# Kernel optimization log

Measured on AMD Instinct MI355X. Metric: run time of the kernel, lower is better.

The kernel has to match this reference:

```python
import jax, jax.numpy as jnp
import numpy as np

S = 4096            # num tokens (single causal sequence)
HID = 1024          # hidden_size
NH = 16             # num query heads
NKV = 4             # num kv heads
HD = 64             # head_dim
THETA = 10000.0
Q_SIZE = NH * HD
KV_SIZE = NKV * HD


def setup_inputs() -> dict:
    key = jax.random.key(0)
    k1, k2, k3 = jax.random.split(key, 3)
    return {
        "positions": jnp.arange(S, dtype=jnp.int32),
        "hidden_states": jax.random.normal(k1, (S, 2 * HID), dtype=jnp.float32),
        "w_qkv": jax.random.normal(k2, (Q_SIZE + 2 * KV_SIZE, 2 * HID), dtype=jnp.float32) * 0.02,
        "w_o": jax.random.normal(k3, (HID, Q_SIZE), dtype=jnp.float32) * 0.02,
    }


def _rope(x, positions):
    # x: [S, H, HD]; neox-style rotate-half RoPE
    half = HD // 2
    inv_freq = 1.0 / (THETA ** (jnp.arange(0, half, dtype=jnp.float32) / half))
    freqs = positions.astype(jnp.float32)[:, None] * inv_freq  # [S, half]
    cos = jnp.cos(freqs)[:, None, :]  # [S, 1, half]
    sin = jnp.sin(freqs)[:, None, :]
    x1, x2 = x[..., :half], x[..., half:]
    return jnp.concatenate([x1 * cos - x2 * sin, x2 * cos + x1 * sin], axis=-1)


def reference(positions, hidden_states, w_qkv, w_o):
    qkv = hidden_states @ w_qkv.T  # [S, Q_SIZE + 2*KV_SIZE]
    q = qkv[:, :Q_SIZE].reshape(S, NH, HD)
    k = qkv[:, Q_SIZE:Q_SIZE + KV_SIZE].reshape(S, NKV, HD)
    v = qkv[:, Q_SIZE + KV_SIZE:].reshape(S, NKV, HD)
    q = _rope(q, positions)
    k = _rope(k, positions)
    # GQA: group query heads over kv heads
    g = NH // NKV
    qg = q.reshape(S, NKV, g, HD)
    scale = HD ** -0.5
    scores = jnp.einsum("qhgd,thd->hgqt", qg, k) * scale  # [NKV, g, S, S]
    causal = positions[:, None] >= positions[None, :]      # [S, S]
    scores = jnp.where(causal[None, None], scores, jnp.finfo(scores.dtype).min)
    probs = jax.nn.softmax(scores, axis=-1)
    o = jnp.einsum("hgqt,thd->qhgd", probs, v).reshape(S, Q_SIZE)
    return o @ w_o.T  # [S, HID]
```

## Files before the change

### kernel.cpp

```cpp
#include <hip/hip_runtime.h>
#include <math.h>

#define S_LEN   4096
#define NHEADS  16
#define NKVH    4
#define HDIM    64
#define QKV_N   1536
#define HID2    2048
#define OUT_N   1024

typedef __attribute__((ext_vector_type(8))) __bf16 bf16x8;
typedef __attribute__((ext_vector_type(4))) __bf16 bf16x4;
typedef __attribute__((ext_vector_type(4))) float  f32x4;
typedef __attribute__((ext_vector_type(16))) float f32x16;
typedef __attribute__((ext_vector_type(4))) unsigned int u32x4;

#define GL_LDS16(gaddr, laddr)                                                  \
  __builtin_amdgcn_global_load_lds(                                             \
      (const __attribute__((address_space(1))) unsigned int*)(gaddr),           \
      (__attribute__((address_space(3))) unsigned int*)(laddr), 16, 0, 0)

__device__ __forceinline__ unsigned cvt_pk_bf16(float lo, float hi) {
  unsigned r;
  asm("v_cvt_pk_bf16_f32 %0, %1, %2" : "=v"(r) : "v"(lo), "v"(hi));
  return r;
}

#define CVT_BLOCKS 6144
__global__ __launch_bounds__(256) void cvt_all(const float* __restrict__ hid,
                                               const float* __restrict__ wq,
                                               const float* __restrict__ wo,
                                               const int* __restrict__ positions,
                                               __bf16* __restrict__ hid_bf,
                                               __bf16* __restrict__ wq_bf,
                                               __bf16* __restrict__ wo_bf,
                                               float* __restrict__ ct,
                                               float* __restrict__ st) {
  if (blockIdx.x < CVT_BLOCKS) {
    const int n1 = S_LEN * HID2;
    const int n2 = QKV_N * HID2;
    int i = (blockIdx.x * blockDim.x + threadIdx.x) * 8;
    const float* src; __bf16* dst; int off;
    if (i < n1)           { src = hid; dst = hid_bf; off = i; }
    else if (i < n1 + n2) { src = wq;  dst = wq_bf;  off = i - n1; }
    else                  { src = wo;  dst = wo_bf;  off = i - n1 - n2; }
    float4 a = *(const float4*)(src + off);
    float4 b = *(const float4*)(src + off + 4);
    bf16x8 o = {(__bf16)a.x,(__bf16)a.y,(__bf16)a.z,(__bf16)a.w,
                (__bf16)b.x,(__bf16)b.y,(__bf16)b.z,(__bf16)b.w};
    *(bf16x8*)(dst + off) = o;
  } else {
    int i = (blockIdx.x - CVT_BLOCKS) * blockDim.x + threadIdx.x;
    int s = i >> 5, d = i & 31;
    double inv = pow(10000.0, -(double)d / 32.0);
    double fr = (double)positions[s] * inv;
    ct[i] = (float)cos(fr);
    st[i] = (float)sin(fr);
  }
}

template<int BM, bool C_BF16>
__global__ __launch_bounds__(256) void gemm_m97(const __bf16* __restrict__ A,
                                                const __bf16* __restrict__ B,
                                                void* __restrict__ Cp,
                                                int M, int N, int K) {
  constexpr int TM = BM / 32;
  __shared__ __align__(16) __bf16 As[BM * 32];
  __shared__ __align__(16) __bf16 Bs[128 * 32];
  const int tid  = threadIdx.x;
  const int bm   = blockIdx.x, bn = blockIdx.y;
  const int wave = tid >> 6, lane = tid & 63;
  const int quad = lane >> 4, col = lane & 15;
  const int wm = (wave >> 1) * (BM / 2), wn = (wave & 1) * 64;

  const int lrow = lane >> 2, lcol = (lane & 3) * 8;
  const __bf16* Ag = A + (size_t)(bm * BM + wave * (BM / 4) + lrow) * K + lcol;
  const __bf16* Bg = B + (size_t)(bn * 128 + wave * 32 + lrow) * K + lcol;
  __bf16* AsW = As + wave * (BM / 4) * 32;
  __bf16* BsW = Bs + wave * 32 * 32;

  f32x4 acc[TM][4];
#pragma unroll
  for (int i = 0; i < TM; ++i)
#pragma unroll
    for (int j = 0; j < 4; ++j) acc[i][j] = (f32x4){0.f, 0.f, 0.f, 0.f};

  for (int kk = 0; kk < K; kk += 32) {
    __syncthreads();
#pragma unroll
    for (int u = 0; u < BM / 64; ++u)
      GL_LDS16(Ag + kk + (size_t)(u * 16) * K, AsW + u * 16 * 32);
    GL_LDS16(Bg + kk,                  BsW);
    GL_LDS16(Bg + kk + (size_t)16 * K, BsW + 16 * 32);
    __syncthreads();

    bf16x8 a[TM], b[4];
#pragma unroll
    for (int tm = 0; tm < TM; ++tm)
      a[tm] = *(const bf16x8*)&As[(wm + tm * 16 + col) * 32 + quad * 8];
#pragma unroll
    for (int tn = 0; tn < 4; ++tn)
      b[tn] = *(const bf16x8*)&Bs[(wn + tn * 16 + col) * 32 + quad * 8];
#pragma unroll
    for (int tm = 0; tm < TM; ++tm)
#pragma unroll
      for (int tn = 0; tn < 4; ++tn)
        acc[tm][tn] = __builtin_amdgcn_mfma_f32_16x16x32_bf16(a[tm], b[tn], acc[tm][tn], 0, 0, 0);
  }

#pragma unroll
  for (int tm = 0; tm < TM; ++tm)
#pragma unroll
    for (int tn = 0; tn < 4; ++tn) {
      int row = bm * BM + wm + tm * 16 + quad * 4;
      int cg  = bn * 128 + wn + tn * 16 + col;
#pragma unroll
      for (int r = 0; r < 4; ++r) {
        if constexpr (C_BF16)
          ((__bf16*)Cp)[(size_t)(row + r) * N + cg] = (__bf16)acc[tm][tn][r];
        else
          ((float*)Cp)[(size_t)(row + r) * N + cg] = acc[tm][tn][r];
      }
    }
}

#define RC_BLOCKS 320
__global__ __launch_bounds__(256) void rope_cast_vt(const __bf16* __restrict__ qkv,
                                                    const float* __restrict__ ct,
                                                    const float* __restrict__ st,
                                                    __bf16* __restrict__ qb,
                                                    __bf16* __restrict__ kb,
                                                    __bf16* __restrict__ vT) {
  if (blockIdx.x < RC_BLOCKS) {
    int g = blockIdx.x * 256 + threadIdx.x;
    int head = g % 20, s = g / 20;
    bool isq = head < NHEADS;
    const __bf16* src = qkv + (size_t)s * QKV_N +
                        (isq ? head * 64 : 1024 + (head - 16) * 64);
    bf16x8 x[8];
#pragma unroll
    for (int u = 0; u < 8; ++u) x[u] = *(const bf16x8*)(src + u * 8);
    float cc[32], ss[32];
#pragma unroll
    for (int u = 0; u < 8; ++u) {
      float4 c4 = *(const float4*)(ct + s * 32 + u * 4);
      float4 s4 = *(const float4*)(st + s * 32 + u * 4);
      cc[4*u] = c4.x; cc[4*u+1] = c4.y; cc[4*u+2] = c4.z; cc[4*u+3] = c4.w;
      ss[4*u] = s4.x; ss[4*u+1] = s4.y; ss[4*u+2] = s4.z; ss[4*u+3] = s4.w;
    }
    const float scl = isq ? 0.18033688011112042f : 1.0f;
    bf16x8 o[8];
#pragma unroll
    for (int d = 0; d < 32; ++d) {
      float x1 = (float)x[d >> 3][d & 7];
      float x2 = (float)x[4 + (d >> 3)][d & 7];
      o[d >> 3][d & 7]       = (__bf16)((x1 * cc[d] - x2 * ss[d]) * scl);
      o[4 + (d >> 3)][d & 7] = (__bf16)((x2 * cc[d] + x1 * ss[d]) * scl);
    }
    __bf16* dst = isq ? (qb + (size_t)s * 1024 + head * 64)
                      : (kb + (size_t)s * 256 + (head - 16) * 64);
#pragma unroll
    for (int u = 0; u < 8; ++u) *(bf16x8*)(dst + u * 8) = o[u];
  } else {
    __shared__ __align__(16) __bf16 Ts[64][72];
    const int idx = blockIdx.x - RC_BLOCKS;
    const int sb = idx & 63, kvh = idx >> 6, t = threadIdx.x;
    const int r = t >> 2, c16 = (t & 3) * 16;
    const __bf16* src = qkv + (size_t)(sb * 64 + r) * QKV_N + 1280 + kvh * 64 + c16;
    bf16x8 v0 = *(const bf16x8*)src;
    bf16x8 v1 = *(const bf16x8*)(src + 8);
#pragma unroll
    for (int u = 0; u < 8; ++u) {
      Ts[c16 + u][r]     = v0[u];
      Ts[c16 + 8 + u][r] = v1[u];
    }
    __syncthreads();
    __bf16* dst = vT + ((size_t)kvh * 64 + r) * S_LEN + sb * 64 + c16;
    *(bf16x8*)dst       = *(const bf16x8*)&Ts[r][c16];
    *(bf16x8*)(dst + 8) = *(const bf16x8*)&Ts[r][c16 + 8];
  }
}

__global__ __launch_bounds__(256, 4) void attn_split(const __bf16* __restrict__ qg,
                                                     const __bf16* __restrict__ kg,
                                                     const __bf16* __restrict__ vg,
                                                     __bf16* __restrict__ op0,
                                                     __bf16* __restrict__ op1,
                                                     __bf16* __restrict__ op2,
                                                     __bf16* __restrict__ op3,
                                                     float* __restrict__ lp) {
  __shared__ __align__(16) __bf16 lds[18432];
  __bf16* Ks = lds;
  __bf16* Vs = lds + 9216;

  const int tid = threadIdx.x;
  const int h = blockIdx.x;
  const int y = 79 - (int)blockIdx.y;
  int qb, c;
  if (y < 8)       { qb = y;                 c = 0; }
  else if (y < 24) { qb = 8  + ((y - 8) >> 1);  c = (y - 8) & 1; }
  else if (y < 48) { qb = 16 + (y - 24) / 3;    c = (y - 24) % 3; }
  else             { qb = 24 + ((y - 48) >> 2); c = (y - 48) & 3; }
  const int n   = 2 * (qb + 1);
  const int nch = (qb >> 3) + 1;
  const int bsz = n / nch, rm = n - bsz * nch;
  const int kt0 = c * bsz + (c < rm ? c : rm);
  const int ktEnd = kt0 + bsz + (c < rm ? 1 : 0);

  const int kvh = h >> 2;
  const int wave = tid >> 6, lane = tid & 63;
  const int r31 = lane & 31, hi = lane >> 5;
  const int hi4 = hi * 4, hi8 = hi * 8;
  const int qbase = qb * 128 + wave * 32;

  {
    const int r = tid >> 1, cc = (tid & 1) * 32;
    const __bf16* src = qg + (size_t)(qb * 128 + r) * 1024 + h * 64 + cc;
    __bf16* dq = lds + r * 72 + cc;
    *(bf16x8*)(dq)      = *(const bf16x8*)(src);
    *(bf16x8*)(dq + 8)  = *(const bf16x8*)(src + 8);
    *(bf16x8*)(dq + 16) = *(const bf16x8*)(src + 16);
    *(bf16x8*)(dq + 24) = *(const bf16x8*)(src + 24);
  }

  const int sr = tid >> 2, sc = (tid & 3) * 16;
  const __bf16* kptr = kg + (size_t)sr * 256 + kvh * 64 + sc;
  const __bf16* vptr = vg + ((size_t)kvh * 64 + sr) * S_LEN + sc;
  bf16x8 kr0 = *(const bf16x8*)(kptr + (size_t)kt0 * 64 * 256);
  bf16x8 kr1 = *(const bf16x8*)(kptr + (size_t)kt0 * 64 * 256 + 8);
  bf16x8 vr0 = *(const bf16x8*)(vptr + (size_t)kt0 * 64);
  bf16x8 vr1 = *(const bf16x8*)(vptr + (size_t)kt0 * 64 + 8);

  __syncthreads();

  bf16x8 qf[4];
#pragma unroll
  for (int dc = 0; dc < 4; ++dc)
    qf[dc] = *(const bf16x8*)&lds[(wave * 32 + r31) * 72 + dc * 16 + hi8];

  __syncthreads();

  f32x16 fz;
#pragma unroll
  for (int g = 0; g < 16; ++g) fz[g] = 0.f;

  f32x16 o[2];
  o[0] = fz; o[1] = fz;
  float lacc = 0.f;

  for (int kt = kt0; kt < ktEnd; ++kt) {
    const int cur = (kt - kt0) & 1;
    {
      __bf16* kd = Ks + cur * 4608 + sr * 72 + sc;
      *(bf16x8*)kd       = kr0;
      *(bf16x8*)(kd + 8) = kr1;
      __bf16* vd = Vs + cur * 4608 + sr * 72 + sc;
      *(bf16x8*)vd       = vr0;
      *(bf16x8*)(vd + 8) = vr1;
    }
    if (kt + 1 < ktEnd) {
      const __bf16* kn = kptr + (size_t)(kt + 1) * 64 * 256;
      const __bf16* vn = vptr + (size_t)(kt + 1) * 64;
      kr0 = *(const bf16x8*)(kn);
      kr1 = *(const bf16x8*)(kn + 8);
      vr0 = *(const bf16x8*)(vn);
      vr1 = *(const bf16x8*)(vn + 8);
    }
    __syncthreads();

    if (kt * 64 > qbase + 31) continue;

    const bool full = (kt * 64 + 63 <= qbase);
    const int thr = qbase + r31 - kt * 64;

    bf16x8 pa[4];
#pragma unroll
    for (int kb = 0; kb < 2; ++kb) {
      bf16x8 kf0 = *(const bf16x8*)&Ks[cur * 4608 + (kb * 32 + r31) * 72 + hi8];
      f32x16 sf = __builtin_amdgcn_mfma_f32_32x32x16_bf16(kf0, qf[0], fz, 0, 0, 0);
#pragma unroll
      for (int dc = 1; dc < 4; ++dc) {
        bf16x8 kf = *(const bf16x8*)&Ks[cur * 4608 + (kb * 32 + r31) * 72 + dc * 16 + hi8];
        sf = __builtin_amdgcn_mfma_f32_32x32x16_bf16(kf, qf[dc], sf, 0, 0, 0);
      }
      float p[16];
#pragma unroll
      for (int g = 0; g < 16; ++g) {
        float e = __builtin_amdgcn_exp2f(sf[g]);
        if (!full) {
          const int krow = kb * 32 + (g & 3) + 8 * (g >> 2) + hi4;
          if (krow > thr) e = 0.f;
        }
        p[g] = e;
      }
#pragma unroll
      for (int m = 0; m < 4; ++m)
        lacc += (p[4 * m] + p[4 * m + 1]) + (p[4 * m + 2] + p[4 * m + 3]);
#pragma unroll
      for (int half = 0; half < 2; ++half) {
        unsigned a0 = cvt_pk_bf16(p[8 * half + 0], p[8 * half + 1]);
        unsigned a1 = cvt_pk_bf16(p[8 * half + 2], p[8 * half + 3]);
        unsigned b0 = cvt_pk_bf16(p[8 * half + 4], p[8 * half + 5]);
        unsigned b1 = cvt_pk_bf16(p[8 * half + 6], p[8 * half + 7]);
        asm("v_permlane32_swap_b32 %0, %1" : "+v"(a0), "+v"(b0));
        asm("v_permlane32_swap_b32 %0, %1" : "+v"(a1), "+v"(b1));
        u32x4 t = {a0, a1, b0, b1};
        pa[kb * 2 + half] = __builtin_bit_cast(bf16x8, t);
      }
    }

#pragma unroll
    for (int dt = 0; dt < 2; ++dt)
#pragma unroll
      for (int kc = 0; kc < 4; ++kc) {
        bf16x8 vf = *(const bf16x8*)&Vs[cur * 4608 + (dt * 32 + r31) * 72 + kc * 16 + hi8];
        o[dt] = __builtin_amdgcn_mfma_f32_32x32x16_bf16(pa[kc], vf, o[dt], 0, 0, 0);
      }
  }

  lacc += __shfl_xor(lacc, 32, 64);
  __syncthreads();
  float* lshw = (float*)lds + wave * 32;
  if (lane < 32) lshw[lane] = lacc;
  asm volatile("s_waitcnt lgkmcnt(0)" ::: "memory");

  __bf16* op = (c == 0) ? op0 : (c == 1) ? op1 : (c == 2) ? op2 : op3;
#pragma unroll
  for (int g = 0; g < 16; ++g) {
    const int rl = (g & 3) + 8 * (g >> 2) + hi4;
    float l = lshw[rl];
    float linv = (l > 0.f) ? 1.f / l : 0.f;
    const size_t row = (size_t)(qb * 128 + wave * 32 + rl);
    op[row * 1024 + h * 64 + r31]      = (__bf16)(o[0][g] * linv);
    op[row * 1024 + h * 64 + 32 + r31] = (__bf16)(o[1][g] * linv);
  }
  if (lane < 32)
    lp[(size_t)(c * S_LEN + qb * 128 + wave * 32 + lane) * NHEADS + h] = lacc;
}

__global__ __launch_bounds__(256) void attn_combine(const __bf16* __restrict__ op0,
                                                    const __bf16* __restrict__ op1,
                                                    const __bf16* __restrict__ op2,
                                                    const __bf16* __restrict__ op3,
                                                    const float* __restrict__ lp,
                                                    __bf16* __restrict__ ob) {
  int i = blockIdx.x * 256 + threadIdx.x;
  int row = i >> 7, c8 = (i & 127) * 8;
  int h = c8 >> 6;
  const int nch = (row >> 10) + 1;
  float l0 = lp[(size_t)row * NHEADS + h];
  float l1 = (nch > 1) ? lp[(size_t)(S_LEN + row) * NHEADS + h] : 0.f;
  float l2 = (nch > 2) ? lp[(size_t)(2 * S_LEN + row) * NHEADS + h] : 0.f;
  float l3 = (nch > 3) ? lp[(size_t)(3 * S_LEN + row) * NHEADS + h] : 0.f;
  float inv = 1.f / (l0 + l1 + l2 + l3);
  float acc[8];
  bf16x8 a = *(const bf16x8*)(op0 + (size_t)row * 1024 + c8);
#pragma unroll
  for (int u = 0; u < 8; ++u) acc[u] = (float)a[u] * l0;
  if (nch > 1) {
    bf16x8 b = *(const bf16x8*)(op1 + (size_t)row * 1024 + c8);
#pragma unroll
    for (int u = 0; u < 8; ++u) acc[u] += (float)b[u] * l1;
  }
  if (nch > 2) {
    bf16x8 b = *(const bf16x8*)(op2 + (size_t)row * 1024 + c8);
#pragma unroll
    for (int u = 0; u < 8; ++u) acc[u] += (float)b[u] * l2;
  }
  if (nch > 3) {
    bf16x8 b = *(const bf16x8*)(op3 + (size_t)row * 1024 + c8);
#pragma unroll
    for (int u = 0; u < 8; ++u) acc[u] += (float)b[u] * l3;
  }
  bf16x8 o;
#pragma unroll
  for (int u = 0; u < 8; ++u) o[u] = (__bf16)(acc[u] * inv);
  *(bf16x8*)(ob + (size_t)row * 1024 + c8) = o;
}

extern "C" void kernel_launch(void* const* d_in, const int* in_sizes, int n_in,
                              void* d_out, int out_size, void* d_ws, size_t ws_size,
                              hipStream_t stream) {
  const int*   positions = (const int*)d_in[0];
  const float* hidden    = (const float*)d_in[1];
  const float* w_qkv     = (const float*)d_in[2];
  const float* w_o       = (const float*)d_in[3];
  float* out = (float*)d_out;

  char* ws = (char*)d_ws;
  __bf16* qkv_bf  = (__bf16*)ws;
  __bf16* Opart0  = (__bf16*)ws;
  __bf16* attn_bf = (__bf16*)ws;
  float*  lpart   = (float*)(ws + 8388608);
  __bf16* hid_bf  = (__bf16*)(ws + 12582912);
  __bf16* q_bf    = (__bf16*)(ws + 12582912);
  __bf16* k_bf    = (__bf16*)(ws + 20971520);
  __bf16* vT      = (__bf16*)(ws + 23068672);
  float*  ct      = (float*)(ws + 29360128);
  float*  st      = (float*)(ws + 29884416);
  __bf16* wq_bf   = (__bf16*)(ws + 30408704);
  __bf16* Opart1  = (__bf16*)(ws + 30408704);
  __bf16* wo_bf   = (__bf16*)(ws + 38797312);
  __bf16* Opart2  = (__bf16*)d_out;
  __bf16* Opart3  = (__bf16*)((char*)d_out + 8388608);

  cvt_all<<<CVT_BLOCKS + S_LEN * 32 / 256, 256, 0, stream>>>(
      hidden, w_qkv, w_o, positions, hid_bf, wq_bf, wo_bf, ct, st);

  gemm_m97<64, true><<<dim3(S_LEN / 64, QKV_N / 128), 256, 0, stream>>>(
      hid_bf, wq_bf, qkv_bf, S_LEN, QKV_N, HID2);

  rope_cast_vt<<<RC_BLOCKS + S_LEN / 64 * NKVH, 256, 0, stream>>>(
      qkv_bf, ct, st, q_bf, k_bf, vT);

  attn_split<<<dim3(NHEADS, 80), 256, 0, stream>>>(q_bf, k_bf, vT,
                                                   Opart0, Opart1, Opart2, Opart3,
                                                   lpart);
  attn_combine<<<S_LEN * 128 / 256, 256, 0, stream>>>(Opart0, Opart1, Opart2, Opart3,
                                                      lpart, attn_bf);

  gemm_m97<64, false><<<dim3(S_LEN / 64, OUT_N / 128), 256, 0, stream>>>(
      attn_bf, wo_bf, out, S_LEN, OUT_N, OUT_N);
}
```

Baseline: 238.1 us.

## Use fixed two-way KV split for attention and larger GEMM row tiles

Replaces the variable 1-4 way causal KV split with a uniform two-way split per query block, ordered so large and small blocks interleave, and simplifies the combine kernel to two partials. Also switches both GEMMs to 128-row tiles. This reduces combine traffic and GEMM block count, at the cost of longer, less balanced attention blocks for late query rows and fewer GEMM blocks for occupancy.

```diff
diff --git a/kernel.cpp b/kernel.cpp
--- a/kernel.cpp
+++ b/kernel.cpp
@@ -186,8 +186,6 @@
                                                      const __bf16* __restrict__ vg,
                                                      __bf16* __restrict__ op0,
                                                      __bf16* __restrict__ op1,
-                                                     __bf16* __restrict__ op2,
-                                                     __bf16* __restrict__ op3,
                                                      float* __restrict__ lp) {
   __shared__ __align__(16) __bf16 lds[18432];
   __bf16* Ks = lds;
@@ -195,28 +193,21 @@
 
   const int tid = threadIdx.x;
   const int h = blockIdx.x;
-  const int y = 79 - (int)blockIdx.y;
-  int qb, c;
-  if (y < 8)       { qb = y;                 c = 0; }
-  else if (y < 24) { qb = 8  + ((y - 8) >> 1);  c = (y - 8) & 1; }
-  else if (y < 48) { qb = 16 + (y - 24) / 3;    c = (y - 24) % 3; }
-  else             { qb = 24 + ((y - 48) >> 2); c = (y - 48) & 3; }
-  const int n   = 2 * (qb + 1);
-  const int nch = (qb >> 3) + 1;
-  const int bsz = n / nch, rm = n - bsz * nch;
-  const int kt0 = c * bsz + (c < rm ? c : rm);
-  const int ktEnd = kt0 + bsz + (c < rm ? 1 : 0);
-
+  const int yy = blockIdx.y;
+  const int qq = yy >> 1, split = yy & 1;
+  const int qb = (qq < 16) ? qq : 47 - qq;
   const int kvh = h >> 2;
   const int wave = tid >> 6, lane = tid & 63;
   const int r31 = lane & 31, hi = lane >> 5;
   const int hi4 = hi * 4, hi8 = hi * 8;
   const int qbase = qb * 128 + wave * 32;
+  const int kt0 = split * (qb + 1);
+  const int ktEnd = kt0 + qb + 1;
 
   {
-    const int r = tid >> 1, cc = (tid & 1) * 32;
-    const __bf16* src = qg + (size_t)(qb * 128 + r) * 1024 + h * 64 + cc;
-    __bf16* dq = lds + r * 72 + cc;
+    const int r = tid >> 1, c = (tid & 1) * 32;
+    const __bf16* src = qg + (size_t)(qb * 128 + r) * 1024 + h * 64 + c;
+    __bf16* dq = lds + r * 72 + c;
     *(bf16x8*)(dq)      = *(const bf16x8*)(src);
     *(bf16x8*)(dq + 8)  = *(const bf16x8*)(src + 8);
     *(bf16x8*)(dq + 16) = *(const bf16x8*)(src + 16);
@@ -324,7 +315,7 @@
   if (lane < 32) lshw[lane] = lacc;
   asm volatile("s_waitcnt lgkmcnt(0)" ::: "memory");
 
-  __bf16* op = (c == 0) ? op0 : (c == 1) ? op1 : (c == 2) ? op2 : op3;
+  __bf16* op = split ? op1 : op0;
 #pragma unroll
   for (int g = 0; g < 16; ++g) {
     const int rl = (g & 3) + 8 * (g >> 2) + hi4;
@@ -335,46 +326,26 @@
     op[row * 1024 + h * 64 + 32 + r31] = (__bf16)(o[1][g] * linv);
   }
   if (lane < 32)
-    lp[(size_t)(c * S_LEN + qb * 128 + wave * 32 + lane) * NHEADS + h] = lacc;
+    lp[(size_t)(split * S_LEN + qb * 128 + wave * 32 + lane) * NHEADS + h] = lacc;
 }
 
 __global__ __launch_bounds__(256) void attn_combine(const __bf16* __restrict__ op0,
                                                     const __bf16* __restrict__ op1,
-                                                    const __bf16* __restrict__ op2,
-                                                    const __bf16* __restrict__ op3,
                                                     const float* __restrict__ lp,
                                                     __bf16* __restrict__ ob) {
   int i = blockIdx.x * 256 + threadIdx.x;
   int row = i >> 7, c8 = (i & 127) * 8;
   int h = c8 >> 6;
-  const int nch = (row >> 10) + 1;
   float l0 = lp[(size_t)row * NHEADS + h];
-  float l1 = (nch > 1) ? lp[(size_t)(S_LEN + row) * NHEADS + h] : 0.f;
-  float l2 = (nch > 2) ? lp[(size_t)(2 * S_LEN + row) * NHEADS + h] : 0.f;
-  float l3 = (nch > 3) ? lp[(size_t)(3 * S_LEN + row) * NHEADS + h] : 0.f;
-  float inv = 1.f / (l0 + l1 + l2 + l3);
-  float acc[8];
+  float l1 = lp[(size_t)(S_LEN + row) * NHEADS + h];
+  float inv = 1.f / (l0 + l1);
+  float w0 = l0 * inv, w1 = l1 * inv;
   bf16x8 a = *(const bf16x8*)(op0 + (size_t)row * 1024 + c8);
-#pragma unroll
-  for (int u = 0; u < 8; ++u) acc[u] = (float)a[u] * l0;
-  if (nch > 1) {
-    bf16x8 b = *(const bf16x8*)(op1 + (size_t)row * 1024 + c8);
-#pragma unroll
-    for (int u = 0; u < 8; ++u) acc[u] += (float)b[u] * l1;
-  }
-  if (nch > 2) {
-    bf16x8 b = *(const bf16x8*)(op2 + (size_t)row * 1024 + c8);
-#pragma unroll
-    for (int u = 0; u < 8; ++u) acc[u] += (float)b[u] * l2;
-  }
-  if (nch > 3) {
-    bf16x8 b = *(const bf16x8*)(op3 + (size_t)row * 1024 + c8);
-#pragma unroll
-    for (int u = 0; u < 8; ++u) acc[u] += (float)b[u] * l3;
-  }
+  bf16x8 b = *(const bf16x8*)(op1 + (size_t)row * 1024 + c8);
   bf16x8 o;
 #pragma unroll
-  for (int u = 0; u < 8; ++u) o[u] = (__bf16)(acc[u] * inv);
+  for (int u = 0; u < 8; ++u)
+    o[u] = (__bf16)((float)a[u] * w0 + (float)b[u] * w1);
   *(bf16x8*)(ob + (size_t)row * 1024 + c8) = o;
 }
 
@@ -401,24 +372,20 @@
   __bf16* wq_bf   = (__bf16*)(ws + 30408704);
   __bf16* Opart1  = (__bf16*)(ws + 30408704);
   __bf16* wo_bf   = (__bf16*)(ws + 38797312);
-  __bf16* Opart2  = (__bf16*)d_out;
-  __bf16* Opart3  = (__bf16*)((char*)d_out + 8388608);
 
   cvt_all<<<CVT_BLOCKS + S_LEN * 32 / 256, 256, 0, stream>>>(
       hidden, w_qkv, w_o, positions, hid_bf, wq_bf, wo_bf, ct, st);
 
-  gemm_m97<64, true><<<dim3(S_LEN / 64, QKV_N / 128), 256, 0, stream>>>(
+  gemm_m97<128, true><<<dim3(S_LEN / 128, QKV_N / 128), 256, 0, stream>>>(
       hid_bf, wq_bf, qkv_bf, S_LEN, QKV_N, HID2);
 
   rope_cast_vt<<<RC_BLOCKS + S_LEN / 64 * NKVH, 256, 0, stream>>>(
       qkv_bf, ct, st, q_bf, k_bf, vT);
 
-  attn_split<<<dim3(NHEADS, 80), 256, 0, stream>>>(q_bf, k_bf, vT,
-                                                   Opart0, Opart1, Opart2, Opart3,
-                                                   lpart);
-  attn_combine<<<S_LEN * 128 / 256, 256, 0, stream>>>(Opart0, Opart1, Opart2, Opart3,
-                                                      lpart, attn_bf);
-
-  gemm_m97<64, false><<<dim3(S_LEN / 64, OUT_N / 128), 256, 0, stream>>>(
+  attn_split<<<dim3(NHEADS, 64), 256, 0, stream>>>(q_bf, k_bf, vT,
+                                                   Opart0, Opart1, lpart);
+  attn_combine<<<S_LEN * 128 / 256, 256, 0, stream>>>(Opart0, Opart1, lpart, attn_bf);
+
+  gemm_m97<128, false><<<dim3(S_LEN / 128, OUT_N / 128), 256, 0, stream>>>(
       attn_bf, wo_bf, out, S_LEN, OUT_N, OUT_N);
 }
```

After: 237.5 us. Within noise of the previous version (-0.3%).
